# Performance work log

Hardware: AMD Instinct MI355X
Metric: run time of the kernel (lower is better)

The kernel has to match this reference:

```python
import jax, jax.numpy as jnp
import numpy as np

WH, WW = 7, 7
NUM_HEADS = 16
DIM = 512
NW = 64  # windows per image (56/7)^2


def _relative_position_index(wh, ww):
    coords = np.stack(np.meshgrid(np.arange(wh), np.arange(ww), indexing='ij'))  # 2,wh,ww
    cf = coords.reshape(2, -1)
    rel = cf[:, :, None] - cf[:, None, :]            # 2,N,N
    rel = rel.transpose(1, 2, 0).astype(np.int32)    # N,N,2
    rel[:, :, 0] += wh - 1
    rel[:, :, 1] += ww - 1
    rel[:, :, 0] *= 2 * ww - 1
    return jnp.asarray(rel.sum(-1))                  # N,N int32


def setup_inputs() -> dict:
    key = jax.random.key(0)
    ks = jax.random.split(key, 7)
    B_, N, C = 2048, WH * WW, DIM
    x = jax.random.normal(ks[0], (B_, N, C), dtype=jnp.float32)
    # 0 / -100 shifted-window mask pattern
    mask = jnp.where(jax.random.uniform(ks[1], (NW, N, N)) < 0.8, 0.0, -100.0).astype(jnp.float32)
    qkv_w = jax.random.normal(ks[2], (3 * C, C), dtype=jnp.float32) * 0.02
    qkv_b = jax.random.normal(ks[3], (3 * C,), dtype=jnp.float32) * 0.02
    proj_w = jax.random.normal(ks[4], (C, C), dtype=jnp.float32) * 0.02
    proj_b = jax.random.normal(ks[5], (C,), dtype=jnp.float32) * 0.02
    rel_bias_table = jax.random.normal(ks[6], ((2 * WH - 1) * (2 * WW - 1), NUM_HEADS), dtype=jnp.float32) * 0.02
    rel_index = _relative_position_index(WH, WW)
    return {"x": x, "mask": mask, "qkv_w": qkv_w, "qkv_b": qkv_b,
            "proj_w": proj_w, "proj_b": proj_b,
            "rel_bias_table": rel_bias_table, "rel_index": rel_index}


def reference(x, mask, qkv_w, qkv_b, proj_w, proj_b, rel_bias_table, rel_index):
    B_, N, C = x.shape
    H = NUM_HEADS
    hd = C // H
    scale = hd ** -0.5
    qkv = x @ qkv_w.T + qkv_b                         # B_,N,3C
    qkv = qkv.reshape(B_, N, 3, H, hd).transpose(2, 0, 3, 1, 4)  # 3,B_,H,N,hd
    q, k, v = qkv[0] * scale, qkv[1], qkv[2]
    attn = jnp.einsum('bhnd,bhmd->bhnm', q, k)        # B_,H,N,N
    # gathered relative position bias -> H,N,N
    bias = rel_bias_table[rel_index.reshape(-1)].reshape(N, N, H).transpose(2, 0, 1)
    attn = attn + bias[None]
    nW = mask.shape[0]
    attn = attn.reshape(B_ // nW, nW, H, N, N) + mask[None, :, None]
    attn = jax.nn.softmax(attn.reshape(B_, H, N, N), axis=-1)
    out = jnp.einsum('bhnm,bhmd->bhnd', attn, v).transpose(0, 2, 1, 3).reshape(B_, N, C)
    return out @ proj_w.T + proj_b
```

## Files before the change

kernel.cpp:

```cpp
#include <hip/hip_runtime.h>

typedef unsigned short u16;
typedef short s16x8 __attribute__((ext_vector_type(8)));
typedef __bf16 bf16x8 __attribute__((ext_vector_type(8)));
typedef float f32x4 __attribute__((ext_vector_type(4)));


__device__ __forceinline__ u16 f2bf(float f) {
  union { float f; unsigned u; } x; x.f = f;
  unsigned r = (x.u + 0x7fffu + ((x.u >> 16) & 1u)) >> 16;
  return (u16)r;
}

__device__ __forceinline__ f32x4 mfma_bf16_16x16x32(s16x8 a, s16x8 b, f32x4 c) {
  return __builtin_amdgcn_mfma_f32_16x16x32_bf16(
      __builtin_bit_cast(bf16x8, a), __builtin_bit_cast(bf16x8, b), c, 0, 0, 0);
}

__device__ __forceinline__ void gl_lds16(const u16* g, u16* l) {
  __builtin_amdgcn_global_load_lds(
      (__attribute__((address_space(1))) unsigned int*)g,
      (__attribute__((address_space(3))) unsigned int*)l, 16, 0, 0);
}


__global__ __launch_bounds__(256) void cvt_bf16(const float* __restrict__ src,
                                                u16* __restrict__ dst, int n) {
  int i = (blockIdx.x * 256 + threadIdx.x) * 4;
  if (i + 3 < n) {
    float4 f = *(const float4*)(src + i);
    ushort4 o;
    o.x = f2bf(f.x); o.y = f2bf(f.y); o.z = f2bf(f.z); o.w = f2bf(f.w);
    *(ushort4*)(dst + i) = o;
  }
}

__global__ __launch_bounds__(256) void build_bias(const float* __restrict__ tbl,
                                                  const int* __restrict__ ridx,
                                                  float* __restrict__ biasf) {
  int t = blockIdx.x * 256 + threadIdx.x;
  if (t < 16 * 2401) {
    int h = t / 2401, ij = t % 2401;
    biasf[t] = tbl[ridx[ij] * 16 + h];
  }
}


template <bool OUT_BF16>
__global__ __launch_bounds__(256) void gemm_bt(const u16* __restrict__ A,
                                               const u16* __restrict__ B,
                                               const float* __restrict__ bias,
                                               void* __restrict__ C,
                                               int M, int N, int K) {
  __shared__ u16 As[128 * 32];
  __shared__ u16 Bs[128 * 32];
  const int t = threadIdx.x;
  const int w = t >> 6, l = t & 63;
  const int quad = l >> 4, lo = l & 15;
  const long m0 = (long)blockIdx.y * 128;
  const long n0 = (long)blockIdx.x * 128;
  const int wm = (w >> 1) * 64, wn = (w & 1) * 64;

  f32x4 acc[4][4] = {};

  const int srow0 = w * 32 + (l >> 2);
  const int skc = (l & 3) * 8;
  const u16* gA = A + (m0 + srow0) * (long)K + skc;
  const u16* gB = B + (n0 + srow0) * (long)K + skc;
  u16* lA = As + (w * 128 + l) * 8;
  u16* lB = Bs + (w * 128 + l) * 8;

  for (int k0 = 0; k0 < K; k0 += 32) {
    gl_lds16(gA + k0, lA);
    gl_lds16(gA + 16 * (long)K + k0, lA + 64 * 8);
    gl_lds16(gB + k0, lB);
    gl_lds16(gB + 16 * (long)K + k0, lB + 64 * 8);
    __syncthreads();

    s16x8 af[4], bfv[4];
#pragma unroll
    for (int i = 0; i < 4; ++i) {
      af[i]  = *(const s16x8*)(As + (wm + i * 16 + lo) * 32 + quad * 8);
      bfv[i] = *(const s16x8*)(Bs + (wn + i * 16 + lo) * 32 + quad * 8);
    }
#pragma unroll
    for (int mt = 0; mt < 4; ++mt)
#pragma unroll
      for (int nt = 0; nt < 4; ++nt)
        acc[mt][nt] = mfma_bf16_16x16x32(af[mt], bfv[nt], acc[mt][nt]);
    __syncthreads();
  }

#pragma unroll
  for (int mt = 0; mt < 4; ++mt) {
#pragma unroll
    for (int nt = 0; nt < 4; ++nt) {
      long col = n0 + wn + nt * 16 + lo;
      float bv = bias[col];
      long rowb = m0 + wm + mt * 16 + quad * 4;
#pragma unroll
      for (int r = 0; r < 4; ++r) {
        float v = acc[mt][nt][r] + bv;
        long off = (rowb + r) * (long)N + col;
        if (OUT_BF16) ((u16*)C)[off] = f2bf(v);
        else          ((float*)C)[off] = v;
      }
    }
  }
}


__global__ __launch_bounds__(256) void attn_kernel(const u16* __restrict__ qkv,
                                                   const float* __restrict__ biasf,
                                                   const float* __restrict__ mask,
                                                   u16* __restrict__ ao) {
  __shared__ u16 P[4][64 * 64];
  const int t = threadIdx.x;
  const int w = t >> 6, l = t & 63;
  const int quad = l >> 4, lo = l & 15;
  const int u = blockIdx.x * 4 + w;
  const int b = u >> 4, h = u & 15;

  const u16* qp = qkv + (long)b * 49 * 1536 + h * 32;
  const u16* kp = qp + 512;
  const u16* vp = qp + 1024;

  const s16x8 zero8 = {};
  s16x8 qf[4], kf[4];
#pragma unroll
  for (int mt = 0; mt < 4; ++mt) {
    int m = mt * 16 + lo;
    qf[mt] = (m < 49) ? *(const s16x8*)(qp + (long)m * 1536 + quad * 8) : zero8;
    kf[mt] = (m < 49) ? *(const s16x8*)(kp + (long)m * 1536 + quad * 8) : zero8;
  }

  f32x4 S[4][4] = {};
#pragma unroll
  for (int mt = 0; mt < 4; ++mt)
#pragma unroll
    for (int nt = 0; nt < 4; ++nt)
      S[mt][nt] = mfma_bf16_16x16x32(qf[mt], kf[nt], S[mt][nt]);

  const float scale = 0.17677669529663687f;
  const float* bh = biasf + h * 2401;
  const float* mw = mask + (long)(b & 63) * 2401;

#pragma unroll
  for (int mt = 0; mt < 4; ++mt) {
#pragma unroll
    for (int r = 0; r < 4; ++r) {
      int row = mt * 16 + quad * 4 + r;
      int rr = row < 49 ? row : 48;
      float vals[4];
#pragma unroll
      for (int nt = 0; nt < 4; ++nt) {
        int col = nt * 16 + lo;
        vals[nt] = (col < 49)
                       ? S[mt][nt][r] * scale + bh[rr * 49 + col] + mw[rr * 49 + col]
                       : -1e30f;
      }
      float rm = fmaxf(fmaxf(vals[0], vals[1]), fmaxf(vals[2], vals[3]));
#pragma unroll
      for (int off = 1; off < 16; off <<= 1) rm = fmaxf(rm, __shfl_xor(rm, off, 16));
      float s = 0.f;
#pragma unroll
      for (int nt = 0; nt < 4; ++nt) {
        vals[nt] = __expf(vals[nt] - rm);
        s += vals[nt];
      }
#pragma unroll
      for (int off = 1; off < 16; off <<= 1) s += __shfl_xor(s, off, 16);
      float is = 1.f / s;
#pragma unroll
      for (int nt = 0; nt < 4; ++nt) S[mt][nt][r] = vals[nt] * is;
    }
  }

  u16* pw = &P[w][0];
#pragma unroll
  for (int mt = 0; mt < 4; ++mt)
#pragma unroll
    for (int nt = 0; nt < 4; ++nt)
#pragma unroll
      for (int r = 0; r < 4; ++r)
        pw[(mt * 16 + quad * 4 + r) * 64 + nt * 16 + lo] = f2bf(S[mt][nt][r]);

  f32x4 O[4][2] = {};
#pragma unroll
  for (int kt = 0; kt < 2; ++kt) {
    s16x8 vb[2];
#pragma unroll
    for (int nt = 0; nt < 2; ++nt) {
      union { u16 us[8]; s16x8 v; } tb;
#pragma unroll
      for (int jj = 0; jj < 8; ++jj) {
        int j = kt * 32 + quad * 8 + jj;
        tb.us[jj] = (j < 49) ? vp[(long)j * 1536 + nt * 16 + lo] : (u16)0;
      }
      vb[nt] = tb.v;
    }
#pragma unroll
    for (int mt = 0; mt < 4; ++mt) {
      s16x8 pa = *(const s16x8*)(pw + (mt * 16 + lo) * 64 + kt * 32 + quad * 8);
      O[mt][0] = mfma_bf16_16x16x32(pa, vb[0], O[mt][0]);
      O[mt][1] = mfma_bf16_16x16x32(pa, vb[1], O[mt][1]);
    }
  }

  u16* op = ao + (long)b * 49 * 512 + h * 32;
#pragma unroll
  for (int mt = 0; mt < 4; ++mt)
#pragma unroll
    for (int nt = 0; nt < 2; ++nt)
#pragma unroll
      for (int r = 0; r < 4; ++r) {
        int row = mt * 16 + quad * 4 + r;
        if (row < 49) op[(long)row * 512 + nt * 16 + lo] = f2bf(O[mt][nt][r]);
      }
}


extern "C" void kernel_launch(void* const* d_in, const int* in_sizes, int n_in,
                              void* d_out, int out_size, void* d_ws, size_t ws_size,
                              hipStream_t stream) {
  const float* x      = (const float*)d_in[0];
  const float* mask   = (const float*)d_in[1];
  const float* qkv_w  = (const float*)d_in[2];
  const float* qkv_b  = (const float*)d_in[3];
  const float* proj_w = (const float*)d_in[4];
  const float* proj_b = (const float*)d_in[5];
  const float* tbl    = (const float*)d_in[6];
  const int*   ridx   = (const int*)d_in[7];

  u16* xb    = (u16*)d_ws;
  u16* qkvb  = xb + 51380224;
  u16* wq    = qkvb + 154140672;
  u16* wp    = wq + 786432;
  float* biasf = (float*)(wp + 262144);

  cvt_bf16<<<50176, 256, 0, stream>>>(x, xb, 51380224);
  cvt_bf16<<<768, 256, 0, stream>>>(qkv_w, wq, 786432);
  cvt_bf16<<<256, 256, 0, stream>>>(proj_w, wp, 262144);
  build_bias<<<151, 256, 0, stream>>>(tbl, ridx, biasf);

  gemm_bt<true><<<dim3(12, 784), 256, 0, stream>>>(xb, wq, qkv_b, qkvb,
                                                   100352, 1536, 512);
  attn_kernel<<<8192, 256, 0, stream>>>(qkvb, biasf, mask, xb);

  gemm_bt<false><<<dim3(4, 784), 256, 0, stream>>>(xb, wp, proj_b, d_out,
                                                   100352, 512, 512);
}
```

Measured before the change: 933.8 us.

## Widen GEMM K-tile with XOR-swizzled LDS, premerge bias+mask, stage V transposed

```diff
diff --git a/kernel.cpp b/kernel.cpp
--- a/kernel.cpp
+++ b/kernel.cpp
@@ -10,6 +10,11 @@
   union { float f; unsigned u; } x; x.f = f;
   unsigned r = (x.u + 0x7fffu + ((x.u >> 16) & 1u)) >> 16;
   return (u16)r;
+}
+
+__device__ __forceinline__ float bf2f(u16 b) {
+  union { unsigned u; float f; } x; x.u = ((unsigned)b) << 16;
+  return x.f;
 }
 
 __device__ __forceinline__ f32x4 mfma_bf16_16x16x32(s16x8 a, s16x8 b, f32x4 c) {
@@ -35,13 +40,16 @@
   }
 }
 
-__global__ __launch_bounds__(256) void build_bias(const float* __restrict__ tbl,
-                                                  const int* __restrict__ ridx,
-                                                  float* __restrict__ biasf) {
+__global__ __launch_bounds__(256) void build_bm(const float* __restrict__ tbl,
+                                                const int* __restrict__ ridx,
+                                                const float* __restrict__ mask,
+                                                u16* __restrict__ bm) {
   int t = blockIdx.x * 256 + threadIdx.x;
-  if (t < 16 * 2401) {
-    int h = t / 2401, ij = t % 2401;
-    biasf[t] = tbl[ridx[ij] * 16 + h];
+  if (t < 64 * 16 * 2401) {
+    int j = t % 2401;
+    int wh = t / 2401;
+    int h = wh & 15, wd = wh >> 4;
+    bm[t] = f2bf(tbl[ridx[j] * 16 + h] + mask[wd * 2401 + j]);
   }
 }
 
@@ -52,8 +60,8 @@
                                                const float* __restrict__ bias,
                                                void* __restrict__ C,
                                                int M, int N, int K) {
-  __shared__ u16 As[128 * 32];
-  __shared__ u16 Bs[128 * 32];
+  __shared__ u16 As[128 * 64];
+  __shared__ u16 Bs[128 * 64];
   const int t = threadIdx.x;
   const int w = t >> 6, l = t & 63;
   const int quad = l >> 4, lo = l & 15;
@@ -63,31 +71,43 @@
 
   f32x4 acc[4][4] = {};
 
-  const int srow0 = w * 32 + (l >> 2);
-  const int skc = (l & 3) * 8;
-  const u16* gA = A + (m0 + srow0) * (long)K + skc;
-  const u16* gB = B + (n0 + srow0) * (long)K + skc;
-  u16* lA = As + (w * 128 + l) * 8;
-  u16* lB = Bs + (w * 128 + l) * 8;
-
-  for (int k0 = 0; k0 < K; k0 += 32) {
-    gl_lds16(gA + k0, lA);
-    gl_lds16(gA + 16 * (long)K + k0, lA + 64 * 8);
-    gl_lds16(gB + k0, lB);
-    gl_lds16(gB + 16 * (long)K + k0, lB + 64 * 8);
+  const u16* gA[4]; const u16* gB[4]; u16* lA[4]; u16* lB[4];
+#pragma unroll
+  for (int i = 0; i < 4; ++i) {
+    int q = i * 256 + t;
+    int row = q >> 3, c = q & 7;
+    int kc = c ^ (row & 7);
+    gA[i] = A + (m0 + row) * (long)K + kc * 8;
+    gB[i] = B + (n0 + row) * (long)K + kc * 8;
+    lA[i] = As + q * 8;
+    lB[i] = Bs + q * 8;
+  }
+
+  for (int k0 = 0; k0 < K; k0 += 64) {
+#pragma unroll
+    for (int i = 0; i < 4; ++i) gl_lds16(gA[i] + k0, lA[i]);
+#pragma unroll
+    for (int i = 0; i < 4; ++i) gl_lds16(gB[i] + k0, lB[i]);
     __syncthreads();
 
-    s16x8 af[4], bfv[4];
-#pragma unroll
-    for (int i = 0; i < 4; ++i) {
-      af[i]  = *(const s16x8*)(As + (wm + i * 16 + lo) * 32 + quad * 8);
-      bfv[i] = *(const s16x8*)(Bs + (wn + i * 16 + lo) * 32 + quad * 8);
-    }
-#pragma unroll
-    for (int mt = 0; mt < 4; ++mt)
-#pragma unroll
-      for (int nt = 0; nt < 4; ++nt)
-        acc[mt][nt] = mfma_bf16_16x16x32(af[mt], bfv[nt], acc[mt][nt]);
+#pragma unroll
+    for (int kk = 0; kk < 2; ++kk) {
+      s16x8 af[4], bfv[4];
+#pragma unroll
+      for (int i = 0; i < 4; ++i) {
+        int ra = wm + i * 16 + lo;
+        int rb = wn + i * 16 + lo;
+        int ca = (kk * 4 + quad) ^ (ra & 7);
+        int cb = (kk * 4 + quad) ^ (rb & 7);
+        af[i]  = *(const s16x8*)(As + (ra * 8 + ca) * 8);
+        bfv[i] = *(const s16x8*)(Bs + (rb * 8 + cb) * 8);
+      }
+#pragma unroll
+      for (int mt = 0; mt < 4; ++mt)
+#pragma unroll
+        for (int nt = 0; nt < 4; ++nt)
+          acc[mt][nt] = mfma_bf16_16x16x32(af[mt], bfv[nt], acc[mt][nt]);
+    }
     __syncthreads();
   }
 
@@ -110,20 +130,34 @@
 }
 
 
-__global__ __launch_bounds__(256) void attn_kernel(const u16* __restrict__ qkv,
-                                                   const float* __restrict__ biasf,
-                                                   const float* __restrict__ mask,
-                                                   u16* __restrict__ ao) {
-  __shared__ u16 P[4][64 * 64];
-  const int t = threadIdx.x;
-  const int w = t >> 6, l = t & 63;
+#define PS 72
+
+__global__ __launch_bounds__(64) void attn_kernel(const u16* __restrict__ qkv,
+                                                  const u16* __restrict__ bm,
+                                                  u16* __restrict__ ao) {
+  __shared__ u16 P[64 * PS];
+  __shared__ u16 VT[32 * PS];
+  const int l = threadIdx.x;
   const int quad = l >> 4, lo = l & 15;
-  const int u = blockIdx.x * 4 + w;
+  const int u = blockIdx.x;
   const int b = u >> 4, h = u & 15;
 
   const u16* qp = qkv + (long)b * 49 * 1536 + h * 32;
   const u16* kp = qp + 512;
   const u16* vp = qp + 1024;
+
+#pragma unroll
+  for (int z = 0; z < 18; ++z) ((unsigned*)VT)[z * 64 + l] = 0;
+
+#pragma unroll
+  for (int rep = 0; rep < 13; ++rep) {
+    int j = rep * 4 + quad;
+    if (j < 49) {
+      unsigned vd = *(const unsigned*)(vp + (long)j * 1536 + lo * 2);
+      VT[(2 * lo) * PS + j] = (u16)vd;
+      VT[(2 * lo + 1) * PS + j] = (u16)(vd >> 16);
+    }
+  }
 
   const s16x8 zero8 = {};
   s16x8 qf[4], kf[4];
@@ -142,8 +176,7 @@
       S[mt][nt] = mfma_bf16_16x16x32(qf[mt], kf[nt], S[mt][nt]);
 
   const float scale = 0.17677669529663687f;
-  const float* bh = biasf + h * 2401;
-  const float* mw = mask + (long)(b & 63) * 2401;
+  const u16* bmp = bm + ((long)(b & 63) * 16 + h) * 2401;
 
 #pragma unroll
   for (int mt = 0; mt < 4; ++mt) {
@@ -156,7 +189,7 @@
       for (int nt = 0; nt < 4; ++nt) {
         int col = nt * 16 + lo;
         vals[nt] = (col < 49)
-                       ? S[mt][nt][r] * scale + bh[rr * 49 + col] + mw[rr * 49 + col]
+                       ? S[mt][nt][r] * scale + bf2f(bmp[rr * 49 + col])
                        : -1e30f;
       }
       float rm = fmaxf(fmaxf(vals[0], vals[1]), fmaxf(vals[2], vals[3]));
@@ -176,34 +209,24 @@
     }
   }
 
-  u16* pw = &P[w][0];
 #pragma unroll
   for (int mt = 0; mt < 4; ++mt)
 #pragma unroll
     for (int nt = 0; nt < 4; ++nt)
 #pragma unroll
       for (int r = 0; r < 4; ++r)
-        pw[(mt * 16 + quad * 4 + r) * 64 + nt * 16 + lo] = f2bf(S[mt][nt][r]);
+        P[(mt * 16 + quad * 4 + r) * PS + nt * 16 + lo] = f2bf(S[mt][nt][r]);
 
   f32x4 O[4][2] = {};
 #pragma unroll
   for (int kt = 0; kt < 2; ++kt) {
-    s16x8 vb[2];
-#pragma unroll
-    for (int nt = 0; nt < 2; ++nt) {
-      union { u16 us[8]; s16x8 v; } tb;
-#pragma unroll
-      for (int jj = 0; jj < 8; ++jj) {
-        int j = kt * 32 + quad * 8 + jj;
-        tb.us[jj] = (j < 49) ? vp[(long)j * 1536 + nt * 16 + lo] : (u16)0;
-      }
-      vb[nt] = tb.v;
-    }
+    s16x8 vb0 = *(const s16x8*)(VT + lo * PS + kt * 32 + quad * 8);
+    s16x8 vb1 = *(const s16x8*)(VT + (16 + lo) * PS + kt * 32 + quad * 8);
 #pragma unroll
     for (int mt = 0; mt < 4; ++mt) {
-      s16x8 pa = *(const s16x8*)(pw + (mt * 16 + lo) * 64 + kt * 32 + quad * 8);
-      O[mt][0] = mfma_bf16_16x16x32(pa, vb[0], O[mt][0]);
-      O[mt][1] = mfma_bf16_16x16x32(pa, vb[1], O[mt][1]);
+      s16x8 pa = *(const s16x8*)(P + (mt * 16 + lo) * PS + kt * 32 + quad * 8);
+      O[mt][0] = mfma_bf16_16x16x32(pa, vb0, O[mt][0]);
+      O[mt][1] = mfma_bf16_16x16x32(pa, vb1, O[mt][1]);
     }
   }
 
@@ -232,20 +255,20 @@
   const float* tbl    = (const float*)d_in[6];
   const int*   ridx   = (const int*)d_in[7];
 
-  u16* xb    = (u16*)d_ws;
-  u16* qkvb  = xb + 51380224;
-  u16* wq    = qkvb + 154140672;
-  u16* wp    = wq + 786432;
-  float* biasf = (float*)(wp + 262144);
+  u16* xb   = (u16*)d_ws;
+  u16* qkvb = xb + 51380224;
+  u16* wq   = qkvb + 154140672;
+  u16* wp   = wq + 786432;
+  u16* bm   = wp + 262144;
 
   cvt_bf16<<<50176, 256, 0, stream>>>(x, xb, 51380224);
   cvt_bf16<<<768, 256, 0, stream>>>(qkv_w, wq, 786432);
   cvt_bf16<<<256, 256, 0, stream>>>(proj_w, wp, 262144);
-  build_bias<<<151, 256, 0, stream>>>(tbl, ridx, biasf);
+  build_bm<<<9604, 256, 0, stream>>>(tbl, ridx, mask, bm);
 
   gemm_bt<true><<<dim3(12, 784), 256, 0, stream>>>(xb, wq, qkv_b, qkvb,
                                                    100352, 1536, 512);
-  attn_kernel<<<8192, 256, 0, stream>>>(qkvb, biasf, mask, xb);
+  attn_kernel<<<32768, 64, 0, stream>>>(qkvb, bm, xb);
 
   gemm_bt<false><<<dim3(4, 784), 256, 0, stream>>>(xb, wp, proj_b, d_out,
                                                    100352, 512, 512);
```

New measurement: 1.043 ms. 11.7% more time.
